# Kernel optimization log

Hardware: AMD Instinct MI355X
Metric: run time of the kernel (lower is better)

The kernel has to match this reference:

```python
import jax, jax.numpy as jnp
import numpy as np

MU = jnp.array([1.0, 0.9, 0.7, 0.5, 0.3, 0.1, -0.1, -0.3, -0.5, -0.7, -0.9], dtype=jnp.float32)
SIGMA = jnp.array([1e-3] + [0.1] * 10, dtype=jnp.float32)
H = 8  # n_head


def _lin(x, W, b):
    return x @ W.T + b


def _knrm_logsum(eq, ed, mq, md):
    # eq:[B,Q,D] ed:[B,L,D] mq:[B,Q] md:[B,L] -> [B,K]
    qn = eq / jnp.maximum(jnp.linalg.norm(eq, axis=2, keepdims=True), 1e-12)
    dn = ed / jnp.maximum(jnp.linalg.norm(ed, axis=2, keepdims=True), 1e-12)
    sim = jnp.einsum('bqe,bde->bqd', qn, dn)
    pv = jnp.exp(-(sim[..., None] - MU) ** 2 / (2.0 * SIGMA ** 2))  # [B,Q,L,K]
    ps = jnp.sum(pv * md[:, None, :, None], axis=2)                 # [B,Q,K]
    lps = jnp.log(jnp.clip(ps, 1e-10, None)) * mq[..., None] * 0.01
    return jnp.sum(lps, axis=1)


def _mha(x, Wq, bq, Wk, bk, Wv, bv, Wo, bo):
    # CyberZHG-style MultiHeadAttention: relu on q/k/v projections and output.
    B, L, D = x.shape
    dh = D // H

    def split(t):
        return t.reshape(B, L, H, dh).transpose(0, 2, 1, 3)

    q = split(jax.nn.relu(_lin(x, Wq, bq)))
    k = split(jax.nn.relu(_lin(x, Wk, bk)))
    v = split(jax.nn.relu(_lin(x, Wv, bv)))
    att = jax.nn.softmax(jnp.einsum('bhqe,bhke->bhqk', q, k) / jnp.sqrt(jnp.float32(dh)), axis=-1)
    y = jnp.einsum('bhqk,bhke->bhqe', att, v).transpose(0, 2, 1, 3).reshape(B, L, D)
    return jax.nn.relu(_lin(y, Wo, bo))


def _forward(masks_q, masks_d, masks_dcq, masks_dbody, emb, Wq, bq, Wk, bk, Wv, bv, Wo, bo,
             tW, tb, qdW, qdb, qbW, qbb, qcqW, qcqb, dcqW, dcqb, bcqW, bcqb,
             expW, expb, combW, combb, inputs_q, inputs_d, inputs_dcq, inputs_dbody):
    eq = emb[inputs_q]
    ed = emb[inputs_d]
    eb = emb[inputs_dbody]
    qd = jnp.tanh(_lin(_knrm_logsum(eq, ed, masks_q, masks_d), qdW, qdb))
    qb = jnp.tanh(_lin(_knrm_logsum(eq, eb, masks_q, masks_dbody), qbW, qbb))
    B, MN, ML = inputs_dcq.shape
    e_dcq = jax.nn.relu(_lin(emb[inputs_dcq.reshape(B, MN * ML)], tW, tb))
    enc_dcq = _mha(e_dcq, Wq, bq, Wk, bk, Wv, bv, Wo, bo).reshape(B, MN, ML, -1)
    enc_d = _mha(ed, Wq, bq, Wk, bk, Wv, bv, Wo, bo)
    enc_b = _mha(eb, Wq, bq, Wk, bk, Wv, bv, Wo, bo)

    def per_cq(i_dcq, m_dcq):  # i_dcq:[B,ML,D] m_dcq:[B,ML]
        return (_knrm_logsum(eq, i_dcq, masks_q, m_dcq),
                _knrm_logsum(enc_d, i_dcq, masks_d, m_dcq),
                _knrm_logsum(enc_b, i_dcq, masks_dbody, m_dcq))

    kq, kd, kb = jax.vmap(per_cq, in_axes=(1, 1))(enc_dcq, masks_dcq)  # [MN,B,K]
    qcqres = jnp.tanh(_lin(kq, qcqW, qcqb))      # [MN,B,1]
    qcqdattn = jnp.tanh(_lin(kd, dcqW, dcqb))
    qcqbattn = jnp.tanh(_lin(kb, bcqW, bcqb))
    qcqd = jnp.sum(qcqres * qcqdattn, axis=0)    # [B,1]
    qcqb2 = jnp.sum(qcqres * qcqbattn, axis=0)
    qcq = _lin(jnp.concatenate([qcqd, qcqb2], axis=1), expW, expb)
    return jnp.tanh(_lin(jnp.concatenate([qd, qb, qcq], axis=1), combW, combb)).squeeze()


def setup_inputs():
    B, Q, DL, BL, MN, ML, D, V = 32, 20, 64, 512, 8, 16, 128, 50000
    key = jax.random.key(0)
    ks = jax.random.split(key, 40)

    def w(i, shape, s=0.05):
        return jax.random.normal(ks[i], shape, jnp.float32) * s

    return {
        'inputs_q': jax.random.randint(ks[0], (B, Q), 1, V),
        'inputs_d': jax.random.randint(ks[1], (B, DL), 1, V),
        'inputs_dcq': jax.random.randint(ks[2], (B, MN, ML), 1, V),
        'inputs_dbody': jax.random.randint(ks[3], (B, BL), 1, V),
        'masks_q': jnp.ones((B, Q), jnp.float32),
        'masks_d': jnp.ones((B, DL), jnp.float32),
        'masks_dcq': jnp.ones((B, MN, ML), jnp.float32),
        'masks_dbody': jnp.ones((B, BL), jnp.float32),
        'emb': w(4, (V, D), 0.1).at[0].set(0.0),  # padding_idx=0
        'Wq': w(5, (D, D)), 'bq': w(6, (D,)),
        'Wk': w(7, (D, D)), 'bk': w(8, (D,)),
        'Wv': w(9, (D, D)), 'bv': w(10, (D,)),
        'Wo': w(11, (D, D)), 'bo': w(12, (D,)),
        'tW': w(13, (D, D)), 'tb': w(14, (D,)),
        'qdW': w(15, (1, 11)), 'qdb': w(16, (1,)),
        'qbW': w(17, (1, 11)), 'qbb': w(18, (1,)),
        'qcqW': w(19, (1, 11)), 'qcqb': w(20, (1,)),
        'dcqW': w(21, (1, 11)), 'dcqb': w(22, (1,)),
        'bcqW': w(23, (1, 11)), 'bcqb': w(24, (1,)),
        'expW': w(25, (1, 2)), 'expb': w(26, (1,)),
        'combW': w(27, (1, 3)), 'combb': w(28, (1,)),
    }


def reference(inputs_q, inputs_d, inputs_dcq, inputs_dbody, masks_q, masks_d, masks_dcq, masks_dbody,
              emb, Wq, bq, Wk, bk, Wv, bv, Wo, bo, tW, tb, qdW, qdb, qbW, qbb, qcqW, qcqb,
              dcqW, dcqb, bcqW, bcqb, expW, expb, combW, combb):
    return _forward(masks_q, masks_d, masks_dcq, masks_dbody, emb, Wq, bq, Wk, bk, Wv, bv, Wo, bo,
                    tW, tb, qdW, qdb, qbW, qbb, qcqW, qcqb, dcqW, dcqb, bcqW, bcqb,
                    expW, expb, combW, combb, inputs_q, inputs_d, inputs_dcq, inputs_dbody)
```

## Files before the change

kernel.cpp:

```cpp
#include <hip/hip_runtime.h>
#include <hip/hip_bf16.h>

#define BB 32
#define QL_ 20
#define DL_ 64
#define BL_ 512
#define MN_ 8
#define ML_ 16
#define DD 128
#define HH 8

#define ROWS_DCQ 4096
#define ROWS_D   2048
#define ROWS_B   16384
#define R_ALL    22528
#define ROWS_EQ  640
#define R_GATHER 23168

typedef float f2 __attribute__((ext_vector_type(2)));

__global__ __launch_bounds__(256) void gather_all(
    const int* __restrict__ in_q, const int* __restrict__ in_d,
    const int* __restrict__ in_dcq, const int* __restrict__ in_db,
    const float* __restrict__ emb, float* __restrict__ x_all, float* __restrict__ ytmp,
    float* __restrict__ inv_eq, float* __restrict__ inv_ed, float* __restrict__ inv_eb,
    float* __restrict__ zero_p, int nzero) {
    int blk = blockIdx.x;
    if (blk >= 2896) {
        int i = (blk - 2896) * 256 + threadIdx.x;
        if (i < nzero) zero_p[i] = 0.f;
        return;
    }
    int t = blk * 256 + threadIdx.x;
    int r = t >> 5, c = t & 31;
    const int* idx; float* outp; float* invp; int lr;
    if (r < ROWS_DCQ)              { idx = in_dcq; outp = ytmp + (size_t)r * DD;  invp = nullptr; lr = r; }
    else if (r < ROWS_DCQ + ROWS_D){ idx = in_d;   outp = x_all + (size_t)r * DD; invp = inv_ed;  lr = r - ROWS_DCQ; }
    else if (r < R_ALL)            { idx = in_db;  outp = x_all + (size_t)r * DD; invp = inv_eb;  lr = r - (ROWS_DCQ + ROWS_D); }
    else                           { idx = in_q;   outp = x_all + (size_t)r * DD; invp = inv_eq;  lr = r - R_ALL; }
    float4 val = ((const float4*)(emb + (size_t)idx[lr] * DD))[c];
    ((float4*)outp)[c] = val;
    float ss = val.x * val.x + val.y * val.y + val.z * val.z + val.w * val.w;
    ss += __shfl_xor(ss, 1, 64);
    ss += __shfl_xor(ss, 2, 64);
    ss += __shfl_xor(ss, 4, 64);
    ss += __shfl_xor(ss, 8, 64);
    ss += __shfl_xor(ss, 16, 64);
    if (c == 0 && invp) invp[lr] = 1.0f / fmaxf(sqrtf(ss), 1e-12f);
}

__device__ __forceinline__ void linear_body(float* __restrict__ wT, float* __restrict__ bs,
                                            const float* __restrict__ in, const float* __restrict__ W,
                                            const float* __restrict__ bias, float* __restrict__ out,
                                            float* __restrict__ inv_out, int block) {
    int t = threadIdx.x;
    for (int i = t; i < DD * DD; i += 256) {
        int o = i >> 7, e = i & 127;
        wT[e * 132 + o] = W[i];
    }
    if (t < 128) bs[t] = bias[t];
    __syncthreads();
    int og = t & 15, rg = t >> 4;
    int rowbase = block * 128 + rg * 8;
    f2 acc[8][4];
#pragma unroll
    for (int r = 0; r < 8; r++)
#pragma unroll
        for (int p = 0; p < 4; p++) acc[r][p] = f2{0.f, 0.f};
    for (int e4 = 0; e4 < 32; e4++) {
        float4 xv[8];
#pragma unroll
        for (int r = 0; r < 8; r++)
            xv[r] = *(const float4*)&in[(size_t)(rowbase + r) * DD + 4 * e4];
#pragma unroll
        for (int ee = 0; ee < 4; ee++) {
            int e = 4 * e4 + ee;
            float4 wa = *(const float4*)&wT[e * 132 + 8 * og];
            float4 wb = *(const float4*)&wT[e * 132 + 8 * og + 4];
            f2 w0 = {wa.x, wa.y}, w1 = {wa.z, wa.w}, w2 = {wb.x, wb.y}, w3 = {wb.z, wb.w};
#pragma unroll
            for (int r = 0; r < 8; r++) {
                float x = ((const float*)&xv[r])[ee];
                f2 x2 = {x, x};
                acc[r][0] = __builtin_elementwise_fma(x2, w0, acc[r][0]);
                acc[r][1] = __builtin_elementwise_fma(x2, w1, acc[r][1]);
                acc[r][2] = __builtin_elementwise_fma(x2, w2, acc[r][2]);
                acc[r][3] = __builtin_elementwise_fma(x2, w3, acc[r][3]);
            }
        }
    }
    float4 ba = *(const float4*)&bs[8 * og];
    float4 bbv = *(const float4*)&bs[8 * og + 4];
    float ss[8];
#pragma unroll
    for (int r = 0; r < 8; r++) {
        float o0 = fmaxf(acc[r][0].x + ba.x, 0.f);
        float o1 = fmaxf(acc[r][0].y + ba.y, 0.f);
        float o2 = fmaxf(acc[r][1].x + ba.z, 0.f);
        float o3 = fmaxf(acc[r][1].y + ba.w, 0.f);
        float o4 = fmaxf(acc[r][2].x + bbv.x, 0.f);
        float o5 = fmaxf(acc[r][2].y + bbv.y, 0.f);
        float o6 = fmaxf(acc[r][3].x + bbv.z, 0.f);
        float o7 = fmaxf(acc[r][3].y + bbv.w, 0.f);
        float4 s1 = {o0, o1, o2, o3}, s2 = {o4, o5, o6, o7};
        float* op = out + (size_t)(rowbase + r) * DD + 8 * og;
        *(float4*)op = s1;
        *(float4*)(op + 4) = s2;
        ss[r] = o0 * o0 + o1 * o1 + o2 * o2 + o3 * o3 + o4 * o4 + o5 * o5 + o6 * o6 + o7 * o7;
    }
    if (inv_out) {
#pragma unroll
        for (int r = 0; r < 8; r++) {
            ss[r] += __shfl_xor(ss[r], 1, 64);
            ss[r] += __shfl_xor(ss[r], 2, 64);
            ss[r] += __shfl_xor(ss[r], 4, 64);
            ss[r] += __shfl_xor(ss[r], 8, 64);
        }
#pragma unroll
        for (int r = 0; r < 8; r++)
            if (og == r) inv_out[rowbase + r] = 1.0f / fmaxf(sqrtf(ss[r]), 1e-12f);
    }
}

__global__ __launch_bounds__(256) void lin_kernel(const float* __restrict__ in, const float* __restrict__ W,
                                                  const float* __restrict__ bias, float* __restrict__ out,
                                                  float* __restrict__ inv_out) {
    __shared__ float wT[DD * 132];
    __shared__ float bs[DD];
    linear_body(wT, bs, in, W, bias, out, inv_out, blockIdx.x);
}

__global__ __launch_bounds__(256) void qkv_all(const float* __restrict__ x,
                                               const float* __restrict__ Wq, const float* __restrict__ bq,
                                               const float* __restrict__ Wk, const float* __restrict__ bk,
                                               const float* __restrict__ Wv, const float* __restrict__ bv,
                                               float* __restrict__ q, float* __restrict__ k, float* __restrict__ v) {
    __shared__ float wT[DD * 132];
    __shared__ float bs[DD];
    int sel = blockIdx.x / 176, blk = blockIdx.x % 176;
    const float* W = (sel == 0) ? Wq : (sel == 1) ? Wk : Wv;
    const float* B = (sel == 0) ? bq : (sel == 1) ? bk : bv;
    float* O = (sel == 0) ? q : (sel == 1) ? k : v;
    linear_body(wT, bs, x, W, B, O, nullptr, blk);
}

__device__ __forceinline__ void attn512_v6(float* __restrict__ sm,
                                           const float* __restrict__ q, const float* __restrict__ k,
                                           const float* __restrict__ v, float* __restrict__ y,
                                           int b, int h) {
    float* ks = sm;
    float* vs = sm + 512 * 16;
    int t = threadIdx.x;
    const size_t base = (size_t)b * 512 * DD + h * 16;
    for (int i = t; i < 512 * 4; i += 512) {
        int j = i >> 2, c = i & 3;
        *(float4*)&ks[j * 16 + 4 * c] = *(const float4*)&k[base + (size_t)j * DD + 4 * c];
        *(float4*)&vs[j * 16 + 4 * c] = *(const float4*)&v[base + (size_t)j * DD + 4 * c];
    }
    int w = t >> 6, lane = t & 63;
    int kg = w & 3, qw = w >> 2;
    int r0 = qw * 256 + lane;
    f2 qv[2][16];
#pragma unroll
    for (int p = 0; p < 2; p++) {
        const float* qa = q + base + (size_t)(r0 + p * 128) * DD;
        const float* qb2 = qa + 64 * DD;
#pragma unroll
        for (int c = 0; c < 4; c++) {
            float4 va = *(const float4*)(qa + 4 * c);
            float4 vb = *(const float4*)(qb2 + 4 * c);
            qv[p][4 * c + 0] = f2{va.x * 0.25f, vb.x * 0.25f};
            qv[p][4 * c + 1] = f2{va.y * 0.25f, vb.y * 0.25f};
            qv[p][4 * c + 2] = f2{va.z * 0.25f, vb.z * 0.25f};
            qv[p][4 * c + 3] = f2{va.w * 0.25f, vb.w * 0.25f};
        }
    }
    f2 acc[2][16];
    f2 l2[2] = {f2{0.f, 0.f}, f2{0.f, 0.f}};
#pragma unroll
    for (int p = 0; p < 2; p++)
#pragma unroll
        for (int e = 0; e < 16; e++) acc[p][e] = f2{0.f, 0.f};
    __syncthreads();
    int j0 = kg * 128;
    for (int j = j0; j < j0 + 128; j++) {
        float kk[16], vv[16];
#pragma unroll
        for (int c = 0; c < 4; c++) {
            *(float4*)&kk[4 * c] = *(const float4*)&ks[j * 16 + 4 * c];
            *(float4*)&vv[4 * c] = *(const float4*)&vs[j * 16 + 4 * c];
        }
        f2 d0a = qv[0][0] * f2{kk[0], kk[0]};
        f2 d1a = qv[0][1] * f2{kk[1], kk[1]};
        f2 d0b = qv[1][0] * f2{kk[0], kk[0]};
        f2 d1b = qv[1][1] * f2{kk[1], kk[1]};
#pragma unroll
        for (int e = 2; e < 16; e += 2) {
            d0a = __builtin_elementwise_fma(qv[0][e], f2{kk[e], kk[e]}, d0a);
            d1a = __builtin_elementwise_fma(qv[0][e + 1], f2{kk[e + 1], kk[e + 1]}, d1a);
            d0b = __builtin_elementwise_fma(qv[1][e], f2{kk[e], kk[e]}, d0b);
            d1b = __builtin_elementwise_fma(qv[1][e + 1], f2{kk[e + 1], kk[e + 1]}, d1b);
        }
        f2 da = d0a + d1a, db = d0b + d1b;
        f2 pa = {__expf(da.x), __expf(da.y)};
        f2 pb = {__expf(db.x), __expf(db.y)};
        l2[0] += pa;
        l2[1] += pb;
#pragma unroll
        for (int e = 0; e < 16; e++) {
            f2 ve = {vv[e], vv[e]};
            acc[0][e] = __builtin_elementwise_fma(pa, ve, acc[0][e]);
            acc[1][e] = __builtin_elementwise_fma(pb, ve, acc[1][e]);
        }
    }
    __syncthreads();
#pragma unroll
    for (int g = 1; g < 4; g++) {
        if (kg == g) {
#pragma unroll
            for (int p = 0; p < 2; p++) {
                int ra = r0 + p * 128;
                float* pa = &sm[ra * 20];
                float* pb = &sm[(ra + 64) * 20];
#pragma unroll
                for (int e = 0; e < 16; e++) { pa[e] = acc[p][e].x; pb[e] = acc[p][e].y; }
                pa[16] = l2[p].x;
                pb[16] = l2[p].y;
            }
        }
        __syncthreads();
        if (kg == 0) {
#pragma unroll
            for (int p = 0; p < 2; p++) {
                int ra = r0 + p * 128;
                const float* pa = &sm[ra * 20];
                const float* pb = &sm[(ra + 64) * 20];
#pragma unroll
                for (int e = 0; e < 16; e++) { acc[p][e].x += pa[e]; acc[p][e].y += pb[e]; }
                l2[p].x += pa[16];
                l2[p].y += pb[16];
            }
        }
        __syncthreads();
    }
    if (kg == 0) {
#pragma unroll
        for (int p = 0; p < 2; p++) {
            float ix = 1.0f / l2[p].x, iy = 1.0f / l2[p].y;
            float o0[16], o1[16];
#pragma unroll
            for (int e = 0; e < 16; e++) { o0[e] = acc[p][e].x * ix; o1[e] = acc[p][e].y * iy; }
            float* yp0 = y + base + (size_t)(r0 + p * 128) * DD;
            float* yp1 = yp0 + 64 * DD;
#pragma unroll
            for (int c = 0; c < 4; c++) {
                *(float4*)(yp0 + 4 * c) = *(const float4*)&o0[4 * c];
                *(float4*)(yp1 + 4 * c) = *(const float4*)&o1[4 * c];
            }
        }
    }
}

template <int L, int NQ>
__device__ __forceinline__ void attn_body(float* __restrict__ sm, const float* __restrict__ q,
                                          const float* __restrict__ k, const float* __restrict__ v,
                                          float* __restrict__ y, int b, int h) {
    constexpr int WAVES = 8;
    constexpr int WQ = L / (32 * NQ);
    constexpr int KG = WAVES / WQ;
    constexpr int KPG = L / KG;
    float* ks = sm;
    float* vs = sm + L * 16;
    int t = threadIdx.x;
    const size_t base = (size_t)b * L * DD + h * 16;
    for (int i = t; i < L * 4; i += 512) {
        int j = i >> 2, c = i & 3;
        *(float4*)&ks[j * 16 + 4 * c] = *(const float4*)&k[base + (size_t)j * DD + 4 * c];
        *(float4*)&vs[j * 16 + 4 * c] = *(const float4*)&v[base + (size_t)j * DD + 4 * c];
    }
    int w = t >> 6, lane = t & 63;
    int ls = lane & 31, eh = lane >> 5;
    int kg = w % KG, qw = w / KG;
    int qb2 = qw * 32 * NQ;
    f2 qv[NQ][4];
#pragma unroll
    for (int n = 0; n < NQ; n++) {
        int qr = qb2 + ls + 32 * n;
        const float* qp = q + base + (size_t)qr * DD + eh * 8;
        float4 a = *(const float4*)qp;
        float4 b4 = *(const float4*)(qp + 4);
        qv[n][0] = f2{a.x, a.y};   qv[n][1] = f2{a.z, a.w};
        qv[n][2] = f2{b4.x, b4.y}; qv[n][3] = f2{b4.z, b4.w};
    }
    f2 acc[NQ][4];
    float l[NQ];
#pragma unroll
    for (int n = 0; n < NQ; n++) {
#pragma unroll
        for (int m = 0; m < 4; m++) acc[n][m] = f2{0.f, 0.f};
        l[n] = 0.f;
    }
    __syncthreads();
    for (int j = kg * KPG; j < (kg + 1) * KPG; j++) {
        float4 ka = *(const float4*)&ks[j * 16 + eh * 8];
        float4 kb2 = *(const float4*)&ks[j * 16 + eh * 8 + 4];
        float4 va = *(const float4*)&vs[j * 16 + eh * 8];
        float4 vb2 = *(const float4*)&vs[j * 16 + eh * 8 + 4];
        f2 kk0 = {ka.x, ka.y}, kk1 = {ka.z, ka.w}, kk2 = {kb2.x, kb2.y}, kk3 = {kb2.z, kb2.w};
        f2 vv0 = {va.x, va.y}, vv1 = {va.z, va.w}, vv2 = {vb2.x, vb2.y}, vv3 = {vb2.z, vb2.w};
#pragma unroll
        for (int n = 0; n < NQ; n++) {
            f2 d2 = qv[n][0] * kk0;
            d2 = __builtin_elementwise_fma(qv[n][1], kk1, d2);
            d2 = __builtin_elementwise_fma(qv[n][2], kk2, d2);
            d2 = __builtin_elementwise_fma(qv[n][3], kk3, d2);
            float sh = d2.x + d2.y;
            float s = sh + __shfl_xor(sh, 32, 64);
            float p = __expf(s * 0.25f);
            l[n] += p;
            f2 p2 = {p, p};
            acc[n][0] = __builtin_elementwise_fma(p2, vv0, acc[n][0]);
            acc[n][1] = __builtin_elementwise_fma(p2, vv1, acc[n][1]);
            acc[n][2] = __builtin_elementwise_fma(p2, vv2, acc[n][2]);
            acc[n][3] = __builtin_elementwise_fma(p2, vv3, acc[n][3]);
        }
    }
    __syncthreads();
    if (kg > 0) {
#pragma unroll
        for (int n = 0; n < NQ; n++) {
            int qr = qb2 + ls + 32 * n;
            float* pp = &sm[((kg - 1) * L + qr) * 20 + eh * 10];
            *(f2*)&pp[0] = acc[n][0];
            *(f2*)&pp[2] = acc[n][1];
            *(f2*)&pp[4] = acc[n][2];
            *(f2*)&pp[6] = acc[n][3];
            pp[8] = l[n];
        }
    }
    __syncthreads();
    if (kg == 0) {
#pragma unroll
        for (int n = 0; n < NQ; n++) {
            int qr = qb2 + ls + 32 * n;
            f2 a0 = acc[n][0], a1 = acc[n][1], a2 = acc[n][2], a3 = acc[n][3];
            float lt = l[n];
#pragma unroll
            for (int g = 1; g < KG; g++) {
                const float* pp = &sm[((g - 1) * L + qr) * 20 + eh * 10];
                a0 += *(const f2*)&pp[0];
                a1 += *(const f2*)&pp[2];
                a2 += *(const f2*)&pp[4];
                a3 += *(const f2*)&pp[6];
                lt += pp[8];
            }
            float inv = 1.0f / lt;
            float4 o1 = {a0.x * inv, a0.y * inv, a1.x * inv, a1.y * inv};
            float4 o2 = {a2.x * inv, a2.y * inv, a3.x * inv, a3.y * inv};
            float* yp = y + base + (size_t)qr * DD + eh * 8;
            *(float4*)yp = o1;
            *(float4*)(yp + 4) = o2;
        }
    }
}

__global__ __launch_bounds__(512, 2) void attn_all(const float* __restrict__ qb_, const float* __restrict__ kb_,
                                                   const float* __restrict__ vb_, float* __restrict__ yb_) {
    __shared__ float sm[16384];
    int blk = blockIdx.x;
    if (blk < 256) {
        const size_t off = (size_t)(ROWS_DCQ + ROWS_D) * DD;
        attn512_v6(sm, qb_ + off, kb_ + off, vb_ + off, yb_ + off, blk & 31, blk >> 5);
    } else if (blk < 512) {
        int local = blk - 256;
        attn_body<128, 1>(sm, qb_, kb_, vb_, yb_, local & 31, local >> 5);
    } else {
        int local = blk - 512;
        const size_t off = (size_t)ROWS_DCQ * DD;
        attn_body<64, 1>(sm, qb_ + off, kb_ + off, vb_ + off, yb_ + off, local & 31, local >> 5);
    }
}

template <int QPT, int DPT, bool RAW>
__device__ void knrm_core(float* __restrict__ sm,
                          const float* __restrict__ Q, const float* __restrict__ invQ,
                          const float* __restrict__ mq, int QL, int q0, int qbase,
                          const float* __restrict__ D, const float* __restrict__ invD,
                          const float* __restrict__ md, int DL, int dbase, int mdbase,
                          float* __restrict__ out) {
    constexpr int QT = QPT * 16, DT = DPT * 16;
    float* qtile = sm;
    float* dtile = qtile + QT * 132;
    float* mdv = dtile + DT * 132;
    float* red = mdv + DT;
    float* outred = red + 4 * 16 * QPT * 11;
    const float MUc[11] = {1.0f, 0.9f, 0.7f, 0.5f, 0.3f, 0.1f, -0.1f, -0.3f, -0.5f, -0.7f, -0.9f};
    const float NC[11]  = {-500000.0f, -50.f, -50.f, -50.f, -50.f, -50.f, -50.f, -50.f, -50.f, -50.f, -50.f};
    int t = threadIdx.x;
    int tq = t & 15, td = t >> 4;
    if (!RAW && t < 11) outred[t] = 0.f;
    for (int i = t; i < QT * 32; i += 256) {
        int r = i >> 5, c = i & 31;
        int qrow = q0 + r;
        float4 val = make_float4(0.f, 0.f, 0.f, 0.f);
        if (qrow < QL) {
            float s = invQ[qbase + qrow];
            float4 g = *(const float4*)(Q + (size_t)(qbase + qrow) * DD + 4 * c);
            val = make_float4(g.x * s, g.y * s, g.z * s, g.w * s);
        }
        *(float4*)&qtile[r * 132 + 4 * c] = val;
    }
    float ps[QPT][11];
#pragma unroll
    for (int i = 0; i < QPT; i++)
#pragma unroll
        for (int kk = 0; kk < 11; kk++) ps[i][kk] = 0.f;

    for (int d0 = 0; d0 < DL; d0 += DT) {
        for (int i = t; i < DT * 32; i += 256) {
            int r = i >> 5, c = i & 31;
            int drow = d0 + r;
            float4 val = make_float4(0.f, 0.f, 0.f, 0.f);
            if (drow < DL) {
                float s = invD[dbase + drow];
                float4 g = *(const float4*)(D + (size_t)(dbase + drow) * DD + 4 * c);
                val = make_float4(g.x * s, g.y * s, g.z * s, g.w * s);
            }
            *(float4*)&dtile[r * 132 + 4 * c] = val;
        }
        if (t < DT) mdv[t] = (d0 + t < DL) ? md[mdbase + d0 + t] : 0.f;
        __syncthreads();
        float dot[QPT][DPT];
#pragma unroll
        for (int i = 0; i < QPT; i++)
#pragma unroll
            for (int j = 0; j < DPT; j++) dot[i][j] = 0.f;
#pragma unroll 2
        for (int e4 = 0; e4 < 32; e4++) {
            float4 qv[QPT], dv[DPT];
#pragma unroll
            for (int i = 0; i < QPT; i++) qv[i] = *(const float4*)&qtile[(tq + 16 * i) * 132 + 4 * e4];
#pragma unroll
            for (int j = 0; j < DPT; j++) dv[j] = *(const float4*)&dtile[(td + 16 * j) * 132 + 4 * e4];
#pragma unroll
            for (int i = 0; i < QPT; i++)
#pragma unroll
                for (int j = 0; j < DPT; j++)
                    dot[i][j] += qv[i].x * dv[j].x + qv[i].y * dv[j].y + qv[i].z * dv[j].z + qv[i].w * dv[j].w;
        }
#pragma unroll
        for (int j = 0; j < DPT; j++) {
            float m = mdv[td + 16 * j];
#pragma unroll
            for (int i = 0; i < QPT; i++) {
                float sim = dot[i][j];
#pragma unroll
                for (int kk = 0; kk < 11; kk++) {
                    float df = sim - MUc[kk];
                    ps[i][kk] = fmaf(__expf(df * df * NC[kk]), m, ps[i][kk]);
                }
            }
        }
        __syncthreads();
    }
#pragma unroll
    for (int i = 0; i < QPT; i++)
#pragma unroll
        for (int kk = 0; kk < 11; kk++) {
            ps[i][kk] += __shfl_xor(ps[i][kk], 16, 64);
            ps[i][kk] += __shfl_xor(ps[i][kk], 32, 64);
        }
    int w = t >> 6;
    if ((t & 63) < 16) {
#pragma unroll
        for (int i = 0; i < QPT; i++)
#pragma unroll
            for (int kk = 0; kk < 11; kk++) red[(w * 16 + tq) * (QPT * 11) + i * 11 + kk] = ps[i][kk];
    }
    __syncthreads();
    for (int i = t; i < 16 * QPT * 11; i += 256) {
        int tq2 = i / (QPT * 11);
        int rem = i - tq2 * (QPT * 11);
        int qi = rem / 11, kk = rem - qi * 11;
        float s = red[(0 * 16 + tq2) * (QPT * 11) + qi * 11 + kk] + red[(1 * 16 + tq2) * (QPT * 11) + qi * 11 + kk]
                + red[(2 * 16 + tq2) * (QPT * 11) + qi * 11 + kk] + red[(3 * 16 + tq2) * (QPT * 11) + qi * 11 + kk];
        int qrow = q0 + tq2 + 16 * qi;
        if (qrow < QL) {
            if (RAW) {
                atomicAdd(&out[qrow * 11 + kk], s);
            } else {
                float lps = logf(fmaxf(s, 1e-10f)) * mq[qbase + qrow] * 0.01f;
                atomicAdd(&outred[kk], lps);
            }
        }
    }
    if (!RAW) {
        __syncthreads();
        if (t < 11) atomicAdd(&out[t], outred[t]);
    }
}

__global__ __launch_bounds__(256) void knrm_all(
    const float* __restrict__ eq, const float* __restrict__ inv_eq, const float* __restrict__ mask_q,
    const float* __restrict__ ed, const float* __restrict__ inv_ed, const float* __restrict__ mask_d,
    const float* __restrict__ eb, const float* __restrict__ inv_eb, const float* __restrict__ mask_db,
    const float* __restrict__ enc_d, const float* __restrict__ inv_encd,
    const float* __restrict__ enc_b, const float* __restrict__ inv_encb,
    const float* __restrict__ enc_dcq, const float* __restrict__ inv_encdcq, const float* __restrict__ mask_dcq,
    float* __restrict__ qdk, float* __restrict__ ps_qb,
    float* __restrict__ kq, float* __restrict__ kd, float* __restrict__ kb) {
    __shared__ float sm[9920];
    int blk = blockIdx.x;
    if (blk < 32) {
        int b = blk;
        knrm_core<2, 2, false>(sm, eq, inv_eq, mask_q, QL_, 0, b * QL_,
                               ed, inv_ed, mask_d, DL_, b * DL_, b * DL_, qdk + b * 11);
    } else if (blk < 544) {
        int u = blk - 32;
        int b = u & 31, ch = u >> 5;
        knrm_core<2, 2, true>(sm, eq, inv_eq, mask_q, QL_, 0, b * QL_,
                              eb, inv_eb, mask_db, 32, b * BL_ + ch * 32, b * BL_ + ch * 32,
                              ps_qb + b * (QL_ * 11));
    } else {
        int u = blk - 544;
        int g = u / 19, sub = u % 19;
        int b = g & 31, inst = g >> 5;
        int dbase = b * (MN_ * ML_) + inst * ML_;
        if (sub == 0)
            knrm_core<2, 1, false>(sm, eq, inv_eq, mask_q, QL_, 0, b * QL_,
                                   enc_dcq, inv_encdcq, mask_dcq, ML_, dbase, dbase,
                                   kq + (size_t)(inst * BB + b) * 11);
        else if (sub < 3)
            knrm_core<2, 1, false>(sm, enc_d, inv_encd, mask_d, DL_, (sub - 1) * 32, b * DL_,
                                   enc_dcq, inv_encdcq, mask_dcq, ML_, dbase, dbase,
                                   kd + (size_t)(inst * BB + b) * 11);
        else
            knrm_core<2, 1, false>(sm, enc_b, inv_encb, mask_db, BL_, (sub - 3) * 32, b * BL_,
                                   enc_dcq, inv_encdcq, mask_dcq, ML_, dbase, dbase,
                                   kb + (size_t)(inst * BB + b) * 11);
    }
}

__device__ inline float dot11(const float* w, const float* x) {
    float s = 0.f;
#pragma unroll
    for (int k = 0; k < 11; k++) s += w[k] * x[k];
    return s;
}

__global__ __launch_bounds__(384) void final_kernel(
    const float* __restrict__ qdk, const float* __restrict__ ps_qb, const float* __restrict__ mask_q,
    const float* __restrict__ kq, const float* __restrict__ kd, const float* __restrict__ kb,
    const float* qdW, const float* qdb, const float* qbW, const float* qbb,
    const float* qcqW, const float* qcqb, const float* dcqW, const float* dcqb,
    const float* bcqW, const float* bcqb, const float* expW, const float* expb,
    const float* combW, const float* combb, float* __restrict__ out) {
    __shared__ float qbk_s[BB * 11];
    int t = threadIdx.x;
    if (t < BB * 11) {
        int b = t / 11, kk = t % 11;
        float s = 0.f;
        for (int qq = 0; qq < QL_; qq++)
            s += logf(fmaxf(ps_qb[b * (QL_ * 11) + qq * 11 + kk], 1e-10f)) * mask_q[b * QL_ + qq];
        qbk_s[t] = s * 0.01f;
    }
    __syncthreads();
    int b = t;
    if (b >= BB) return;
    float qd = tanhf(dot11(qdW, qdk + b * 11) + qdb[0]);
    float qb = tanhf(dot11(qbW, qbk_s + b * 11) + qbb[0]);
    float qcqd = 0.f, qcqb2 = 0.f;
    for (int i = 0; i < MN_; i++) {
        int base = (i * BB + b) * 11;
        float r  = tanhf(dot11(qcqW, kq + base) + qcqb[0]);
        float da = tanhf(dot11(dcqW, kd + base) + dcqb[0]);
        float ba = tanhf(dot11(bcqW, kb + base) + bcqb[0]);
        qcqd += r * da;
        qcqb2 += r * ba;
    }
    float qcq = expW[0] * qcqd + expW[1] * qcqb2 + expb[0];
    out[b] = tanhf(combW[0] * qd + combW[1] * qb + combW[2] * qcq + combb[0]);
}

extern "C" void kernel_launch(void* const* d_in, const int* in_sizes, int n_in,
                              void* d_out, int out_size, void* d_ws, size_t ws_size,
                              hipStream_t stream) {
    const int*   in_q    = (const int*)d_in[0];
    const int*   in_d    = (const int*)d_in[1];
    const int*   in_dcq  = (const int*)d_in[2];
    const int*   in_db   = (const int*)d_in[3];
    const float* mask_q  = (const float*)d_in[4];
    const float* mask_d  = (const float*)d_in[5];
    const float* mask_dcq= (const float*)d_in[6];
    const float* mask_db = (const float*)d_in[7];
    const float* emb     = (const float*)d_in[8];
    const float* Wq = (const float*)d_in[9];   const float* bq = (const float*)d_in[10];
    const float* Wk = (const float*)d_in[11];  const float* bk = (const float*)d_in[12];
    const float* Wv = (const float*)d_in[13];  const float* bv = (const float*)d_in[14];
    const float* Wo = (const float*)d_in[15];  const float* bo = (const float*)d_in[16];
    const float* tW = (const float*)d_in[17];  const float* tb = (const float*)d_in[18];
    const float* qdW = (const float*)d_in[19]; const float* qdb = (const float*)d_in[20];
    const float* qbW = (const float*)d_in[21]; const float* qbb = (const float*)d_in[22];
    const float* qcqW = (const float*)d_in[23];const float* qcqb = (const float*)d_in[24];
    const float* dcqW = (const float*)d_in[25];const float* dcqb = (const float*)d_in[26];
    const float* bcqW = (const float*)d_in[27];const float* bcqb = (const float*)d_in[28];
    const float* expW = (const float*)d_in[29];const float* expb = (const float*)d_in[30];
    const float* combW = (const float*)d_in[31];const float* combb = (const float*)d_in[32];
    float* out = (float*)d_out;

    float* ws = (float*)d_ws;
    size_t off = 0;
    auto alloc = [&](size_t n) { float* p = ws + off; off += n; return p; };
    float* x_all = alloc((size_t)R_GATHER * DD);
    float* qbuf  = alloc((size_t)R_ALL * DD);
    float* kbuf  = alloc((size_t)R_ALL * DD);
    float* vbuf  = alloc((size_t)R_ALL * DD);
    float* inv_eq  = alloc(ROWS_EQ);
    float* inv_ed  = alloc(ROWS_D);
    float* inv_eb  = alloc(ROWS_B);
    float* inv_enc = alloc(R_ALL);
    float* qdk   = alloc(BB * 11);
    float* kq    = alloc(MN_ * BB * 11);
    float* kd    = alloc(MN_ * BB * 11);
    float* kb    = alloc(MN_ * BB * 11);
    float* ps_qb = alloc(BB * QL_ * 11);
    (void)ws_size; (void)in_sizes; (void)n_in; (void)out_size;
    const int kZeroCount = BB * 11 + 3 * MN_ * BB * 11 + BB * QL_ * 11;

    const float* eq      = x_all + (size_t)R_ALL * DD;
    const float* ed      = x_all + (size_t)ROWS_DCQ * DD;
    const float* eb      = x_all + (size_t)(ROWS_DCQ + ROWS_D) * DD;
    float* enc_all = kbuf;
    const float* enc_dcq = enc_all;
    const float* enc_d   = enc_all + (size_t)ROWS_DCQ * DD;
    const float* enc_b   = enc_all + (size_t)(ROWS_DCQ + ROWS_D) * DD;
    const float* inv_encdcq = inv_enc;
    const float* inv_encd   = inv_enc + ROWS_DCQ;
    const float* inv_encb   = inv_enc + ROWS_DCQ + ROWS_D;

    gather_all<<<2896 + (kZeroCount + 255) / 256, 256, 0, stream>>>(in_q, in_d, in_dcq, in_db, emb,
                                                                    x_all, kbuf, inv_eq, inv_ed, inv_eb,
                                                                    qdk, kZeroCount);
    lin_kernel<<<ROWS_DCQ / 128, 256, 0, stream>>>(kbuf, tW, tb, x_all, nullptr);
    qkv_all<<<3 * (R_ALL / 128), 256, 0, stream>>>(x_all, Wq, bq, Wk, bk, Wv, bv, qbuf, kbuf, vbuf);
    attn_all<<<768, 512, 0, stream>>>(qbuf, kbuf, vbuf, qbuf);
    lin_kernel<<<R_ALL / 128, 256, 0, stream>>>(qbuf, Wo, bo, enc_all, inv_enc);
    knrm_all<<<5408, 256, 0, stream>>>(eq, inv_eq, mask_q, ed, inv_ed, mask_d, eb, inv_eb, mask_db,
                                       enc_d, inv_encd, enc_b, inv_encb, enc_dcq, inv_encdcq, mask_dcq,
                                       qdk, ps_qb, kq, kd, kb);
    final_kernel<<<1, 384, 0, stream>>>(qdk, ps_qb, mask_q, kq, kd, kb,
                                        qdW, qdb, qbW, qbb, qcqW, qcqb, dcqW, dcqb,
                                        bcqW, bcqb, expW, expb, combW, combb, out);
}
```

Before: 355.3 us.

## Stream V from global in 512-attention and fuse final kernel into knrm via counter

The long-sequence attention path no longer stages V in shared memory and loads V rows directly from global memory each iteration, shrinking its LDS footprint and tightening the partial-sum stride. Separately, the final scalar reduction kernel is folded into knrm_all using an atomic completion counter, so the last block to finish computes the output, removing one launch. Risks: per-iteration global V loads add latency in the inner loop, and the last-block pattern depends on the counter being zeroed each call.

```diff
diff --git a/kernel.cpp b/kernel.cpp
--- a/kernel.cpp
+++ b/kernel.cpp
@@ -144,18 +144,16 @@
     linear_body(wT, bs, x, W, B, O, nullptr, blk);
 }
 
-__device__ __forceinline__ void attn512_v6(float* __restrict__ sm,
+__device__ __forceinline__ void attn512_v8(float* __restrict__ sm,
                                            const float* __restrict__ q, const float* __restrict__ k,
                                            const float* __restrict__ v, float* __restrict__ y,
                                            int b, int h) {
     float* ks = sm;
-    float* vs = sm + 512 * 16;
     int t = threadIdx.x;
     const size_t base = (size_t)b * 512 * DD + h * 16;
     for (int i = t; i < 512 * 4; i += 512) {
         int j = i >> 2, c = i & 3;
         *(float4*)&ks[j * 16 + 4 * c] = *(const float4*)&k[base + (size_t)j * DD + 4 * c];
-        *(float4*)&vs[j * 16 + 4 * c] = *(const float4*)&v[base + (size_t)j * DD + 4 * c];
     }
     int w = t >> 6, lane = t & 63;
     int kg = w & 3, qw = w >> 2;
@@ -184,11 +182,12 @@
     __syncthreads();
     int j0 = kg * 128;
     for (int j = j0; j < j0 + 128; j++) {
+        const float* vp = v + base + (size_t)j * DD;
         float kk[16], vv[16];
 #pragma unroll
         for (int c = 0; c < 4; c++) {
             *(float4*)&kk[4 * c] = *(const float4*)&ks[j * 16 + 4 * c];
-            *(float4*)&vv[4 * c] = *(const float4*)&vs[j * 16 + 4 * c];
+            *(float4*)&vv[4 * c] = *(const float4*)(vp + 4 * c);
         }
         f2 d0a = qv[0][0] * f2{kk[0], kk[0]};
         f2 d1a = qv[0][1] * f2{kk[1], kk[1]};
@@ -220,8 +219,8 @@
 #pragma unroll
             for (int p = 0; p < 2; p++) {
                 int ra = r0 + p * 128;
-                float* pa = &sm[ra * 20];
-                float* pb = &sm[(ra + 64) * 20];
+                float* pa = &sm[ra * 17];
+                float* pb = &sm[(ra + 64) * 17];
 #pragma unroll
                 for (int e = 0; e < 16; e++) { pa[e] = acc[p][e].x; pb[e] = acc[p][e].y; }
                 pa[16] = l2[p].x;
@@ -233,8 +232,8 @@
 #pragma unroll
             for (int p = 0; p < 2; p++) {
                 int ra = r0 + p * 128;
-                const float* pa = &sm[ra * 20];
-                const float* pb = &sm[(ra + 64) * 20];
+                const float* pa = &sm[ra * 17];
+                const float* pb = &sm[(ra + 64) * 17];
 #pragma unroll
                 for (int e = 0; e < 16; e++) { acc[p][e].x += pa[e]; acc[p][e].y += pb[e]; }
                 l2[p].x += pa[16];
@@ -366,11 +365,11 @@
 
 __global__ __launch_bounds__(512, 2) void attn_all(const float* __restrict__ qb_, const float* __restrict__ kb_,
                                                    const float* __restrict__ vb_, float* __restrict__ yb_) {
-    __shared__ float sm[16384];
+    __shared__ float sm[8704];
     int blk = blockIdx.x;
     if (blk < 256) {
         const size_t off = (size_t)(ROWS_DCQ + ROWS_D) * DD;
-        attn512_v6(sm, qb_ + off, kb_ + off, vb_ + off, yb_ + off, blk & 31, blk >> 5);
+        attn512_v8(sm, qb_ + off, kb_ + off, vb_ + off, yb_ + off, blk & 31, blk >> 5);
     } else if (blk < 512) {
         int local = blk - 256;
         attn_body<128, 1>(sm, qb_, kb_, vb_, yb_, local & 31, local >> 5);
@@ -500,6 +499,13 @@
     }
 }
 
+__device__ inline float dot11(const float* w, const float* x) {
+    float s = 0.f;
+#pragma unroll
+    for (int k = 0; k < 11; k++) s += w[k] * x[k];
+    return s;
+}
+
 __global__ __launch_bounds__(256) void knrm_all(
     const float* __restrict__ eq, const float* __restrict__ inv_eq, const float* __restrict__ mask_q,
     const float* __restrict__ ed, const float* __restrict__ inv_ed, const float* __restrict__ mask_d,
@@ -508,7 +514,12 @@
     const float* __restrict__ enc_b, const float* __restrict__ inv_encb,
     const float* __restrict__ enc_dcq, const float* __restrict__ inv_encdcq, const float* __restrict__ mask_dcq,
     float* __restrict__ qdk, float* __restrict__ ps_qb,
-    float* __restrict__ kq, float* __restrict__ kd, float* __restrict__ kb) {
+    float* __restrict__ kq, float* __restrict__ kd, float* __restrict__ kb,
+    int* __restrict__ counter,
+    const float* qdW, const float* qdb, const float* qbW, const float* qbb,
+    const float* qcqW, const float* qcqb, const float* dcqW, const float* dcqb,
+    const float* bcqW, const float* bcqb, const float* expW, const float* expb,
+    const float* combW, const float* combb, float* __restrict__ out) {
     __shared__ float sm[9920];
     int blk = blockIdx.x;
     if (blk < 32) {
@@ -539,30 +550,20 @@
                                    enc_dcq, inv_encdcq, mask_dcq, ML_, dbase, dbase,
                                    kb + (size_t)(inst * BB + b) * 11);
     }
-}
-
-__device__ inline float dot11(const float* w, const float* x) {
-    float s = 0.f;
-#pragma unroll
-    for (int k = 0; k < 11; k++) s += w[k] * x[k];
-    return s;
-}
-
-__global__ __launch_bounds__(384) void final_kernel(
-    const float* __restrict__ qdk, const float* __restrict__ ps_qb, const float* __restrict__ mask_q,
-    const float* __restrict__ kq, const float* __restrict__ kd, const float* __restrict__ kb,
-    const float* qdW, const float* qdb, const float* qbW, const float* qbb,
-    const float* qcqW, const float* qcqb, const float* dcqW, const float* dcqb,
-    const float* bcqW, const float* bcqb, const float* expW, const float* expb,
-    const float* combW, const float* combb, float* __restrict__ out) {
-    __shared__ float qbk_s[BB * 11];
+    __threadfence();
+    __shared__ int lastflag;
     int t = threadIdx.x;
-    if (t < BB * 11) {
-        int b = t / 11, kk = t % 11;
+    if (t == 0) lastflag = atomicAdd(counter, 1);
+    __syncthreads();
+    if (lastflag != (int)gridDim.x - 1) return;
+    __threadfence();
+    float* qbk_s = sm;
+    for (int i = t; i < BB * 11; i += 256) {
+        int b = i / 11, kk = i % 11;
         float s = 0.f;
         for (int qq = 0; qq < QL_; qq++)
             s += logf(fmaxf(ps_qb[b * (QL_ * 11) + qq * 11 + kk], 1e-10f)) * mask_q[b * QL_ + qq];
-        qbk_s[t] = s * 0.01f;
+        qbk_s[i] = s * 0.01f;
     }
     __syncthreads();
     int b = t;
@@ -624,8 +625,9 @@
     float* kd    = alloc(MN_ * BB * 11);
     float* kb    = alloc(MN_ * BB * 11);
     float* ps_qb = alloc(BB * QL_ * 11);
+    int*   counter = (int*)alloc(1);
     (void)ws_size; (void)in_sizes; (void)n_in; (void)out_size;
-    const int kZeroCount = BB * 11 + 3 * MN_ * BB * 11 + BB * QL_ * 11;
+    const int kZeroCount = BB * 11 + 3 * MN_ * BB * 11 + BB * QL_ * 11 + 1;
 
     const float* eq      = x_all + (size_t)R_ALL * DD;
     const float* ed      = x_all + (size_t)ROWS_DCQ * DD;
@@ -647,8 +649,7 @@
     lin_kernel<<<R_ALL / 128, 256, 0, stream>>>(qbuf, Wo, bo, enc_all, inv_enc);
     knrm_all<<<5408, 256, 0, stream>>>(eq, inv_eq, mask_q, ed, inv_ed, mask_d, eb, inv_eb, mask_db,
                                        enc_d, inv_encd, enc_b, inv_encb, enc_dcq, inv_encdcq, mask_dcq,
-                                       qdk, ps_qb, kq, kd, kb);
-    final_kernel<<<1, 384, 0, stream>>>(qdk, ps_qb, mask_q, kq, kd, kb,
-                                        qdW, qdb, qbW, qbb, qcqW, qcqb, dcqW, dcqb,
-                                        bcqW, bcqb, expW, expb, combW, combb, out);
-}
+                                       qdk, ps_qb, kq, kd, kb, counter,
+                                       qdW, qdb, qbW, qbb, qcqW, qcqb, dcqW, dcqb,
+                                       bcqW, bcqb, expW, expb, combW, combb, out);
+}
```

Result: slower. 659.5 us (+85.6%).
